# Kernel optimization log

Hardware: AMD Instinct MI355X
Metric: run time of the kernel (lower is better)

Reference implementation:

```python
import jax, jax.numpy as jnp
import numpy as np

NHEAD = 8
D_K = 64
BETA = 2.0
MIN_RBF = 0.01
MAX_RBF = 0.99
MIN_SPREAD, MAX_SPREAD, BASE, NUM_SPREAD = 1.0, 6.0, 20.0, 8
LN_EPS = 1e-5


def _spreads():
    # torch: min + (max-min) * (logspace(0,1,num,base) - 1) / (base - 1)
    return MIN_SPREAD + (MAX_SPREAD - MIN_SPREAD) * (BASE ** jnp.linspace(0.0, 1.0, NUM_SPREAD) - 1.0) / (BASE - 1.0)


def _layernorm(x, g, b):
    m = jnp.mean(x, axis=-1, keepdims=True)
    v = jnp.mean((x - m) ** 2, axis=-1, keepdims=True)
    return (x - m) * jax.lax.rsqrt(v + LN_EPS) * g + b


def setup_inputs() -> dict:
    key = jax.random.key(0)
    ks = jax.random.split(key, 12)
    B, N, D, H, K, DH = 4, 1024, 512, NHEAD, D_K, 1024
    s = 0.05
    return {
        "x": jax.random.normal(ks[0], (B, N, D), jnp.float32),
        "coords": jax.random.normal(ks[1], (B, N, 3), jnp.float32) * 8.0,  # Angstrom-scale spread
        "q_proj": jax.random.normal(ks[2], (H, D, K), jnp.float32) * s,
        "k_proj": jax.random.normal(ks[3], (H, D, K), jnp.float32) * s,
        "v_proj": jax.random.normal(ks[4], (H, D, K), jnp.float32) * s,
        "q_bias": jnp.zeros((H, K), jnp.float32),
        "k_bias": jnp.zeros((H, K), jnp.float32),
        "v_bias": jnp.zeros((H, K), jnp.float32),
        "w_out": jax.random.normal(ks[5], (D, D), jnp.float32) * s,
        "ln1_g": jnp.ones((D,), jnp.float32),
        "ln1_b": jnp.zeros((D,), jnp.float32),
        "w1": jax.random.normal(ks[6], (DH, D), jnp.float32) * s,
        "b1": jnp.zeros((DH,), jnp.float32),
        "w2": jax.random.normal(ks[7], (D, DH), jnp.float32) * s,
        "b2": jnp.zeros((D,), jnp.float32),
        "ln2_g": jnp.ones((D,), jnp.float32),
        "ln2_b": jnp.zeros((D,), jnp.float32),
    }


def reference(x, coords, q_proj, k_proj, v_proj, q_bias, k_bias, v_bias,
              w_out, ln1_g, ln1_b, w1, b1, w2, b2, ln2_g, ln2_b):
    B, N, D = x.shape
    # per-head QKV projections: [B,H,N,K]
    Q = jnp.einsum('bnd,hdk->bhnk', x, q_proj) + q_bias[None, :, None, :]
    K_ = jnp.einsum('bnd,hdk->bhnk', x, k_proj) + k_bias[None, :, None, :]
    V = jnp.einsum('bnd,hdk->bhnk', x, v_proj) + v_bias[None, :, None, :]

    S = jnp.einsum('bhnk,bhmk->bhnm', Q, K_) / np.float32(np.sqrt(D_K))

    # pairwise squared distances [B,N,N] and per-head gaussian RBFs [B,H,N,N]
    d2 = jnp.sum((coords[:, :, None, :] - coords[:, None, :, :]) ** 2, axis=-1)
    spreads = _spreads().astype(x.dtype)  # [H]
    rbf = jnp.exp(-d2[:, None, :, :] / (2.0 * spreads[None, :, None, None] ** 2))
    valid = (rbf >= MIN_RBF) & (rbf <= MAX_RBF)  # sparse attention band

    # probs proportional to exp(S) * rbf**beta, restricted to the valid band
    logits = jnp.where(valid, S + BETA * jnp.log(jnp.maximum(rbf, 1e-12)), -1e9)
    p = jax.nn.softmax(logits, axis=-1)
    p = jnp.where(valid, p, 0.0)  # fully-masked rows -> zero output

    o = jnp.einsum('bhnm,bhmk->bhnk', p, V)
    # torch: out.permute(0,2,3,1).reshape(B,N,D) -> interleave (d_k, head)
    o = o.transpose(0, 2, 3, 1).reshape(B, N, D)
    attn_out = o @ w_out.T

    x = _layernorm(x + attn_out, ln1_g, ln1_b)
    h = jax.nn.gelu(x @ w1.T + b1)
    ffn = h @ w2.T + b2
    x = _layernorm(x + ffn, ln2_g, ln2_b)
    return x
```

## Files before the change

kernel.cpp:

```cpp
#include <hip/hip_runtime.h>
#include <cmath>

typedef short s16x8 __attribute__((ext_vector_type(8)));
typedef float f32x4 __attribute__((ext_vector_type(4)));
typedef unsigned short u16;

#define MFMA(a, b, c) __builtin_amdgcn_mfma_f32_16x16x32_bf16((a), (b), (c), 0, 0, 0)
#define NEG_INF (-__builtin_inff())

__device__ inline u16 f2b(float f) {
    union { float f; unsigned u; } v; v.f = f;
    unsigned r = v.u + 0x7fffu + ((v.u >> 16) & 1u);
    return (u16)(r >> 16);
}

__device__ inline void glds16(const u16* g, u16* l) {
    __builtin_amdgcn_global_load_lds(
        (const __attribute__((address_space(1))) unsigned int*)g,
        (__attribute__((address_space(3))) unsigned int*)l, 16, 0, 0);
}

__global__ __launch_bounds__(256) void prep_kernel(
    const float* __restrict__ x,
    const float* __restrict__ qp, const float* __restrict__ kp, const float* __restrict__ vp,
    const float* __restrict__ w_out, const float* __restrict__ w1, const float* __restrict__ w2,
    u16* __restrict__ xb, u16* __restrict__ Bqkv, u16* __restrict__ w_outp,
    u16* __restrict__ w1b, u16* __restrict__ w2b)
{
    const int NXV = 262144;
    const int NQKV = 786432;
    const int NWO = 262144;
    const int NW1 = 524288;
    const int NW2 = 524288;
    const int TOT = NXV + NQKV + NWO + NW1 + NW2;
    for (int i = blockIdx.x * 256 + threadIdx.x; i < TOT; i += gridDim.x * 256) {
        int j = i;
        if (j < NXV) {
            const int base = j * 8;
            float4 a0 = *(const float4*)(x + base);
            float4 a1 = *(const float4*)(x + base + 4);
            s16x8 o;
            o[0]=f2b(a0.x); o[1]=f2b(a0.y); o[2]=f2b(a0.z); o[3]=f2b(a0.w);
            o[4]=f2b(a1.x); o[5]=f2b(a1.y); o[6]=f2b(a1.z); o[7]=f2b(a1.w);
            *(s16x8*)(xb + base) = o;
            continue;
        }
        j -= NXV;
        if (j < NQKV) {
            const int k = j & 63, d = (j >> 6) & 511, zh = j >> 15;
            const int z = zh >> 3, h = zh & 7;
            const float* W = (z == 0) ? qp : (z == 1) ? kp : vp;
            const float v = W[h * 32768 + d * 64 + k];
            Bqkv[(z * 512 + h * 64 + k) * 512 + d] = f2b(v);
            continue;
        }
        j -= NQKV;
        if (j < NWO) {
            const int oc = j & 511, row = j >> 9;
            const int h = oc >> 6, k = oc & 63;
            w_outp[j] = f2b(w_out[row * 512 + k * 8 + h]);
            continue;
        }
        j -= NWO;
        if (j < NW1) { w1b[j] = f2b(w1[j]); continue; }
        j -= NW1;
        w2b[j] = f2b(w2[j]);
    }
}

template<int TM>
__device__ inline void gemm_core(const u16* __restrict__ A, const u16* __restrict__ B,
                                 int K, int ktiles, int kstart, int r0, int c0,
                                 u16* As, u16* Bs, f32x4 (&acc)[TM / 32][4])
{
    const int t = threadIdx.x, lane = t & 63, wid = t >> 6;
    const int l15 = lane & 15, lg = lane >> 4, sw = l15 & 7;
    constexpr int FR = TM / 32;
    const int wr = (wid & 1) * (TM / 2), wc = (wid >> 1) * 64;
    constexpr int NA = TM * 8 / 256;

    const f32x4 zero = {0.f, 0.f, 0.f, 0.f};
    #pragma unroll
    for (int fr = 0; fr < FR; ++fr)
        #pragma unroll
        for (int fc = 0; fc < 4; ++fc) acc[fr][fc] = zero;

    for (int kt = 0; kt < ktiles; ++kt) {
        const int k0 = kstart + kt * 64;
        __syncthreads();
        #pragma unroll
        for (int i = 0; i < NA; ++i) {
            const int slot = i * 256 + t;
            const int row = slot >> 3, c = slot & 7;
            glds16(A + (size_t)(r0 + row) * K + k0 + ((c ^ (row & 7)) << 3),
                   As + i * 2048 + wid * 512);
        }
        #pragma unroll
        for (int i = 0; i < 4; ++i) {
            const int slot = i * 256 + t;
            const int row = slot >> 3, c = slot & 7;
            glds16(B + (size_t)(c0 + row) * K + k0 + ((c ^ (row & 7)) << 3),
                   Bs + i * 2048 + wid * 512);
        }
        __syncthreads();
        #pragma unroll
        for (int ks = 0; ks < 2; ++ks) {
            const int cc = ((ks * 4 + lg) ^ sw) * 8;
            s16x8 af[FR], bf[4];
            #pragma unroll
            for (int f = 0; f < FR; ++f)
                af[f] = *(const s16x8*)(As + (wr + f * 16 + l15) * 64 + cc);
            #pragma unroll
            for (int f = 0; f < 4; ++f)
                bf[f] = *(const s16x8*)(Bs + (wc + f * 16 + l15) * 64 + cc);
            #pragma unroll
            for (int fr = 0; fr < FR; ++fr)
                #pragma unroll
                for (int fc = 0; fc < 4; ++fc)
                    acc[fr][fc] = MFMA(af[fr], bf[fc], acc[fr][fc]);
        }
    }
}

__global__ __launch_bounds__(256) void gemm_qkv_kernel(
    const u16* __restrict__ xb, const u16* __restrict__ Bqkv,
    const float* __restrict__ qb, const float* __restrict__ kb, const float* __restrict__ vb,
    u16* __restrict__ Qb, u16* __restrict__ Kb, u16* __restrict__ Vtb)
{
    __shared__ __align__(16) u16 As[64 * 64];
    __shared__ __align__(16) u16 Bs[128 * 64];
    f32x4 acc[2][4];
    const int r0 = blockIdx.x * 64, c0 = blockIdx.y * 128;
    gemm_core<64>(xb, Bqkv, 512, 8, 0, r0, c0, As, Bs, acc);

    const int t = threadIdx.x, lane = t & 63, wid = t >> 6;
    const int wr = (wid & 1) * 32, wc = (wid >> 1) * 64;
    const int l15 = lane & 15, lg = lane >> 4;

    #pragma unroll
    for (int fc = 0; fc < 4; ++fc) {
        const int gc = c0 + wc + fc * 16 + l15;
        const int z = gc >> 9;
        const int hk = gc & 511;
        const int h = hk >> 6, k = gc & 63;
        const float bias = (z == 0 ? qb : z == 1 ? kb : vb)[hk];
        #pragma unroll
        for (int fr = 0; fr < 2; ++fr) {
            #pragma unroll
            for (int r = 0; r < 4; ++r) {
                const int grow = r0 + wr + fr * 16 + lg * 4 + r;
                const int b = grow >> 10, n = grow & 1023;
                const int bh = b * 8 + h;
                const u16 val = f2b(acc[fr][fc][r] + bias);
                if (z == 0)      Qb[(size_t)bh * 65536 + n * 64 + k] = val;
                else if (z == 1) Kb[(size_t)bh * 65536 + n * 64 + k] = val;
                else             Vtb[(size_t)bh * 65536 + k * 1024 + n] = val;
            }
        }
    }
}

template<int EPI>
__global__ __launch_bounds__(256) void gemm_kernel(
    const u16* __restrict__ A, const u16* __restrict__ B, const float* __restrict__ bias,
    float* __restrict__ Cf, u16* __restrict__ Cb, int N, int K, int ktiles, size_t pstride)
{
    __shared__ __align__(16) u16 As[64 * 64];
    __shared__ __align__(16) u16 Bs[128 * 64];
    f32x4 acc[2][4];
    const int r0 = blockIdx.x * 64, c0 = blockIdx.y * 128;
    const int kstart = blockIdx.z * ktiles * 64;
    gemm_core<64>(A, B, K, ktiles, kstart, r0, c0, As, Bs, acc);
    float* Cfz = Cf + (size_t)blockIdx.z * pstride;

    const int t = threadIdx.x, lane = t & 63, wid = t >> 6;
    const int wr = (wid & 1) * 32, wc = (wid >> 1) * 64;
    const int l15 = lane & 15, lg = lane >> 4;

    #pragma unroll
    for (int fc = 0; fc < 4; ++fc) {
        const int gc = c0 + wc + fc * 16 + l15;
        const float bv = (EPI == 2) ? bias[gc] : 0.f;
        #pragma unroll
        for (int fr = 0; fr < 2; ++fr) {
            #pragma unroll
            for (int r = 0; r < 4; ++r) {
                const int grow = r0 + wr + fr * 16 + lg * 4 + r;
                float v = acc[fr][fc][r] + bv;
                if (EPI == 2) {
                    const float u = 0.7978845608028654f * (v + 0.044715f * v * v * v);
                    v = 0.5f * v * (1.0f + tanhf(u));
                    Cb[(size_t)grow * N + gc] = f2b(v);
                } else {
                    Cfz[(size_t)grow * N + gc] = v;
                }
            }
        }
    }
}

struct AttnParams { float g[8], lo[8], hi[8]; };

__global__ __launch_bounds__(256) void attn_kernel(
    const u16* __restrict__ Qb, const u16* __restrict__ Kb, const u16* __restrict__ Vtb,
    const float* __restrict__ coords, u16* __restrict__ Ob, AttnParams prm)
{
    __shared__ float cmx[1024], cmy[1024], cmz[1024];
    __shared__ __align__(16) u16 Ps[4][16][72];

    const int wg = blockIdx.x;
    const int swz = (wg & 7) * 64 + (wg >> 3);
    const int bh = swz >> 4;
    const int n0 = (swz & 15) * 64;
    const int b = bh >> 3, h = bh & 7;
    const float g = prm.g[h], lo = prm.lo[h], hi = prm.hi[h];

    const int t = threadIdx.x, lane = t & 63, wid = t >> 6;
    const int l15 = lane & 15, lg = lane >> 4;
    const int wq0 = wid * 16;

    for (int i = t; i < 1024; i += 256) {
        const float* c = coords + ((size_t)b * 1024 + i) * 3;
        cmx[i] = c[0]; cmy[i] = c[1]; cmz[i] = c[2];
    }
    __syncthreads();

    s16x8 qf[2];
    {
        const u16* qp_ = Qb + (size_t)bh * 65536 + (size_t)(n0 + wq0 + l15) * 64;
        qf[0] = *(const s16x8*)(qp_ + lg * 8);
        qf[1] = *(const s16x8*)(qp_ + 32 + lg * 8);
    }
    float qx[4], qy[4], qz[4];
    #pragma unroll
    for (int r = 0; r < 4; ++r) {
        const int qn = n0 + wq0 + lg * 4 + r;
        qx[r] = cmx[qn]; qy[r] = cmy[qn]; qz[r] = cmz[qn];
    }

    float m_run[4], l_run[4];
    f32x4 o_acc[4];
    const f32x4 zero = {0.f, 0.f, 0.f, 0.f};
    #pragma unroll
    for (int r = 0; r < 4; ++r) { m_run[r] = NEG_INF; l_run[r] = 0.f; }
    #pragma unroll
    for (int kf = 0; kf < 4; ++kf) o_acc[kf] = zero;

    const u16* Kbh = Kb + (size_t)bh * 65536;
    const u16* Vbh = Vtb + (size_t)bh * 65536;

    for (int mt = 0; mt < 16; ++mt) {
        const int m0 = mt * 64;

        f32x4 s[4];
        #pragma unroll
        for (int mf = 0; mf < 4; ++mf) {
            const u16* kp_ = Kbh + (size_t)(m0 + mf * 16 + l15) * 64;
            s16x8 kf0 = *(const s16x8*)(kp_ + lg * 8);
            s16x8 kf1 = *(const s16x8*)(kp_ + 32 + lg * 8);
            f32x4 a = zero;
            a = MFMA(qf[0], kf0, a);
            a = MFMA(qf[1], kf1, a);
            s[mf] = a;
        }

        s16x8 vfr[2][4];
        #pragma unroll
        for (int ms = 0; ms < 2; ++ms)
            #pragma unroll
            for (int kf = 0; kf < 4; ++kf)
                vfr[ms][kf] = *(const s16x8*)(Vbh + (size_t)(kf * 16 + l15) * 1024
                                              + m0 + ms * 32 + lg * 8);

        float p[4][4];
        float tmax[4] = {NEG_INF, NEG_INF, NEG_INF, NEG_INF};
        #pragma unroll
        for (int mf = 0; mf < 4; ++mf) {
            const int mloc = m0 + mf * 16 + l15;
            const float mx = cmx[mloc], my = cmy[mloc], mz = cmz[mloc];
            #pragma unroll
            for (int r = 0; r < 4; ++r) {
                const float dx = qx[r] - mx, dy = qy[r] - my, dz = qz[r] - mz;
                const float d2 = fmaf(dx, dx, fmaf(dy, dy, dz * dz));
                const bool valid = (d2 >= lo) && (d2 <= hi);
                const float lgt = fmaf(s[mf][r], 0.125f, d2 * g);
                const float v = valid ? lgt : NEG_INF;
                p[mf][r] = v;
                tmax[r] = fmaxf(tmax[r], v);
            }
        }
        #pragma unroll
        for (int r = 0; r < 4; ++r) {
            float v = tmax[r];
            v = fmaxf(v, __shfl_xor(v, 1));
            v = fmaxf(v, __shfl_xor(v, 2));
            v = fmaxf(v, __shfl_xor(v, 4));
            v = fmaxf(v, __shfl_xor(v, 8));
            const float mnew = fmaxf(m_run[r], v);
            const float scale = (mnew == NEG_INF) ? 1.f : __expf(m_run[r] - mnew);
            m_run[r] = mnew;
            float rs = 0.f;
            #pragma unroll
            for (int mf = 0; mf < 4; ++mf) {
                const float pv = (p[mf][r] == NEG_INF) ? 0.f : __expf(p[mf][r] - mnew);
                p[mf][r] = pv;
                rs += pv;
            }
            rs += __shfl_xor(rs, 1); rs += __shfl_xor(rs, 2);
            rs += __shfl_xor(rs, 4); rs += __shfl_xor(rs, 8);
            l_run[r] = l_run[r] * scale + rs;
            #pragma unroll
            for (int kf = 0; kf < 4; ++kf) o_acc[kf][r] *= scale;
        }

        #pragma unroll
        for (int mf = 0; mf < 4; ++mf)
            #pragma unroll
            for (int r = 0; r < 4; ++r)
                Ps[wid][lg * 4 + r][mf * 16 + l15] = f2b(p[mf][r]);

        #pragma unroll
        for (int ms = 0; ms < 2; ++ms) {
            s16x8 pa = *(const s16x8*)&Ps[wid][l15][ms * 32 + lg * 8];
            #pragma unroll
            for (int kf = 0; kf < 4; ++kf)
                o_acc[kf] = MFMA(pa, vfr[ms][kf], o_acc[kf]);
        }
    }

    #pragma unroll
    for (int kf = 0; kf < 4; ++kf) {
        #pragma unroll
        for (int r = 0; r < 4; ++r) {
            const int n = n0 + wq0 + lg * 4 + r;
            const float invl = (l_run[r] > 0.f) ? 1.f / l_run[r] : 0.f;
            Ob[((size_t)b * 1024 + n) * 512 + h * 64 + kf * 16 + l15] = f2b(o_acc[kf][r] * invl);
        }
    }
}

template<int NSRC, bool CB, bool WB16>
__global__ __launch_bounds__(256) void add_ln_kernel(
    const float* __restrict__ a, const float* __restrict__ b0, const float* __restrict__ b1,
    const float* __restrict__ cb, const float* __restrict__ g, const float* __restrict__ bt,
    float* __restrict__ out, u16* __restrict__ outb)
{
    const int lane = threadIdx.x & 63;
    const int row = blockIdx.x * 4 + (threadIdx.x >> 6);
    const size_t base = (size_t)row * 512 + lane * 8;

    float v[8];
    {
        float4 a0 = *(const float4*)(a + base);
        float4 a1 = *(const float4*)(a + base + 4);
        float4 p0 = *(const float4*)(b0 + base);
        float4 p1 = *(const float4*)(b0 + base + 4);
        v[0]=a0.x+p0.x; v[1]=a0.y+p0.y; v[2]=a0.z+p0.z; v[3]=a0.w+p0.w;
        v[4]=a1.x+p1.x; v[5]=a1.y+p1.y; v[6]=a1.z+p1.z; v[7]=a1.w+p1.w;
        if (NSRC == 3) {
            float4 q0 = *(const float4*)(b1 + base);
            float4 q1 = *(const float4*)(b1 + base + 4);
            v[0]+=q0.x; v[1]+=q0.y; v[2]+=q0.z; v[3]+=q0.w;
            v[4]+=q1.x; v[5]+=q1.y; v[6]+=q1.z; v[7]+=q1.w;
        }
        if (CB) {
            float4 c0 = *(const float4*)(cb + lane * 8);
            float4 c1 = *(const float4*)(cb + lane * 8 + 4);
            v[0]+=c0.x; v[1]+=c0.y; v[2]+=c0.z; v[3]+=c0.w;
            v[4]+=c1.x; v[5]+=c1.y; v[6]+=c1.z; v[7]+=c1.w;
        }
    }
    float s = 0.f;
    #pragma unroll
    for (int k = 0; k < 8; ++k) s += v[k];
    #pragma unroll
    for (int m = 1; m <= 32; m <<= 1) s += __shfl_xor(s, m);
    const float mean = s * (1.0f / 512.0f);

    float vs = 0.f;
    #pragma unroll
    for (int k = 0; k < 8; ++k) { const float d = v[k] - mean; vs += d * d; }
    #pragma unroll
    for (int m = 1; m <= 32; m <<= 1) vs += __shfl_xor(vs, m);
    const float rstd = rsqrtf(vs * (1.0f / 512.0f) + 1e-5f);

    float4 g0 = *(const float4*)(g + lane * 8);
    float4 g1 = *(const float4*)(g + lane * 8 + 4);
    float4 t0 = *(const float4*)(bt + lane * 8);
    float4 t1 = *(const float4*)(bt + lane * 8 + 4);
    float gg[8] = {g0.x,g0.y,g0.z,g0.w,g1.x,g1.y,g1.z,g1.w};
    float tb[8] = {t0.x,t0.y,t0.z,t0.w,t1.x,t1.y,t1.z,t1.w};

    float o[8];
    #pragma unroll
    for (int k = 0; k < 8; ++k) o[k] = (v[k] - mean) * rstd * gg[k] + tb[k];
    float4 w0; w0.x=o[0]; w0.y=o[1]; w0.z=o[2]; w0.w=o[3];
    float4 w1; w1.x=o[4]; w1.y=o[5]; w1.z=o[6]; w1.w=o[7];
    *(float4*)(out + base) = w0;
    *(float4*)(out + base + 4) = w1;
    if (WB16) {
        s16x8 q;
        #pragma unroll
        for (int k = 0; k < 8; ++k) q[k] = (short)f2b(o[k]);
        *(s16x8*)(outb + base) = q;
    }
}

extern "C" void kernel_launch(void* const* d_in, const int* in_sizes, int n_in,
                              void* d_out, int out_size, void* d_ws, size_t ws_size,
                              hipStream_t stream)
{
    const float* x      = (const float*)d_in[0];
    const float* coords = (const float*)d_in[1];
    const float* qp     = (const float*)d_in[2];
    const float* kp     = (const float*)d_in[3];
    const float* vp     = (const float*)d_in[4];
    const float* qbias  = (const float*)d_in[5];
    const float* kbias  = (const float*)d_in[6];
    const float* vbias  = (const float*)d_in[7];
    const float* w_out  = (const float*)d_in[8];
    const float* ln1g   = (const float*)d_in[9];
    const float* ln1b   = (const float*)d_in[10];
    const float* w1     = (const float*)d_in[11];
    const float* b1     = (const float*)d_in[12];
    const float* w2     = (const float*)d_in[13];
    const float* b2     = (const float*)d_in[14];
    const float* ln2g   = (const float*)d_in[15];
    const float* ln2b   = (const float*)d_in[16];
    float* out = (float*)d_out;

    char* W = (char*)d_ws;
    u16*  xb     = (u16*)(W + 0);
    u16*  Bqkv   = (u16*)(W + 4194304);
    u16*  w_outp = (u16*)(W + 5767168);
    u16*  w1b    = (u16*)(W + 6291456);
    u16*  w2b    = (u16*)(W + 7340032);
    u16*  Qb     = (u16*)(W + 8388608);
    u16*  Kb     = (u16*)(W + 12582912);
    u16*  Vtb    = (u16*)(W + 16777216);
    u16*  Ob     = (u16*)(W + 20971520);
    float* X1    = (float*)(W + 25165824);
    u16*  Hb     = (u16*)(W + 33554432);
    float* P0    = (float*)(W + 41943040);
    float* P1    = P0 + 2097152;
    u16*  X1b    = Qb;

    AttnParams prm;
    for (int h = 0; h < 8; ++h) {
        const double sg = 1.0 + 5.0 * (pow(20.0, (double)h / 7.0) - 1.0) / 19.0;
        const double s2 = sg * sg;
        prm.g[h]  = (float)(-1.0 / s2);
        prm.lo[h] = (float)(2.0 * s2 * log(100.0 / 99.0));
        prm.hi[h] = (float)(2.0 * s2 * log(100.0));
    }

    prep_kernel<<<1024, 256, 0, stream>>>(x, qp, kp, vp, w_out, w1, w2,
                                          xb, Bqkv, w_outp, w1b, w2b);
    gemm_qkv_kernel<<<dim3(64, 12), 256, 0, stream>>>(xb, Bqkv, qbias, kbias, vbias,
                                                      Qb, Kb, Vtb);
    attn_kernel<<<512, 256, 0, stream>>>(Qb, Kb, Vtb, coords, Ob, prm);
    gemm_kernel<0><<<dim3(64, 4, 2), 256, 0, stream>>>(Ob, w_outp, nullptr, P0, nullptr,
                                                       512, 512, 4, 2097152);
    add_ln_kernel<3, false, true><<<1024, 256, 0, stream>>>(x, P0, P1, nullptr,
                                                            ln1g, ln1b, X1, X1b);
    gemm_kernel<2><<<dim3(64, 8), 256, 0, stream>>>(X1b, w1b, b1, nullptr, Hb,
                                                    1024, 512, 8, 0);
    gemm_kernel<0><<<dim3(64, 4, 2), 256, 0, stream>>>(Hb, w2b, nullptr, P0, nullptr,
                                                       512, 1024, 8, 2097152);
    add_ln_kernel<3, true, false><<<1024, 256, 0, stream>>>(X1, P0, P1, b2,
                                                            ln2g, ln2b, out, nullptr);
}
```

Measured before the change: 138.7 us.

## Split attention over key halves, drop online-max softmax, enlarge GEMM tiles

The attention kernel is split into two key-range halves, which doubles the block count to 1024. Each half writes unnormalised fp32 partial outputs and row sums, and a new merge kernel combines them into bf16. The online running-max softmax is replaced by exp2 with a fixed offset of -8, and the 1/sqrt(dk)·log2e scale is folded into Q in the QKV GEMM epilogue. This removes the per-tile max reductions, rescaling and shuffles. Separately, all GEMMs move from 64-row to 128-row tiles (4x4 MFMA fragments per wave), which gives more reuse but halves the grid. The fixed-offset softmax relies on logits staying in a bounded range and may overflow or underflow for larger-magnitude inputs. The split adds an extra kernel and fp32 partial traffic.

New measurement: 166.8 us. 20.2% more time.

```diff
diff --git a/kernel.cpp b/kernel.cpp
--- a/kernel.cpp
+++ b/kernel.cpp
@@ -68,20 +68,17 @@
     }
 }
 
-template<int TM>
 __device__ inline void gemm_core(const u16* __restrict__ A, const u16* __restrict__ B,
                                  int K, int ktiles, int kstart, int r0, int c0,
-                                 u16* As, u16* Bs, f32x4 (&acc)[TM / 32][4])
+                                 u16* As, u16* Bs, f32x4 (&acc)[4][4])
 {
     const int t = threadIdx.x, lane = t & 63, wid = t >> 6;
     const int l15 = lane & 15, lg = lane >> 4, sw = l15 & 7;
-    constexpr int FR = TM / 32;
-    const int wr = (wid & 1) * (TM / 2), wc = (wid >> 1) * 64;
-    constexpr int NA = TM * 8 / 256;
+    const int wr = (wid & 1) * 64, wc = (wid >> 1) * 64;
 
     const f32x4 zero = {0.f, 0.f, 0.f, 0.f};
     #pragma unroll
-    for (int fr = 0; fr < FR; ++fr)
+    for (int fr = 0; fr < 4; ++fr)
         #pragma unroll
         for (int fc = 0; fc < 4; ++fc) acc[fr][fc] = zero;
 
@@ -89,7 +86,7 @@
         const int k0 = kstart + kt * 64;
         __syncthreads();
         #pragma unroll
-        for (int i = 0; i < NA; ++i) {
+        for (int i = 0; i < 4; ++i) {
             const int slot = i * 256 + t;
             const int row = slot >> 3, c = slot & 7;
             glds16(A + (size_t)(r0 + row) * K + k0 + ((c ^ (row & 7)) << 3),
@@ -106,15 +103,15 @@
         #pragma unroll
         for (int ks = 0; ks < 2; ++ks) {
             const int cc = ((ks * 4 + lg) ^ sw) * 8;
-            s16x8 af[FR], bf[4];
-            #pragma unroll
-            for (int f = 0; f < FR; ++f)
+            s16x8 af[4], bf[4];
+            #pragma unroll
+            for (int f = 0; f < 4; ++f)
                 af[f] = *(const s16x8*)(As + (wr + f * 16 + l15) * 64 + cc);
             #pragma unroll
             for (int f = 0; f < 4; ++f)
                 bf[f] = *(const s16x8*)(Bs + (wc + f * 16 + l15) * 64 + cc);
             #pragma unroll
-            for (int fr = 0; fr < FR; ++fr)
+            for (int fr = 0; fr < 4; ++fr)
                 #pragma unroll
                 for (int fc = 0; fc < 4; ++fc)
                     acc[fr][fc] = MFMA(af[fr], bf[fc], acc[fr][fc]);
@@ -122,19 +119,20 @@
     }
 }
 
+#define SCALE_Q 0.18033688f
 __global__ __launch_bounds__(256) void gemm_qkv_kernel(
     const u16* __restrict__ xb, const u16* __restrict__ Bqkv,
     const float* __restrict__ qb, const float* __restrict__ kb, const float* __restrict__ vb,
     u16* __restrict__ Qb, u16* __restrict__ Kb, u16* __restrict__ Vtb)
 {
-    __shared__ __align__(16) u16 As[64 * 64];
+    __shared__ __align__(16) u16 As[128 * 64];
     __shared__ __align__(16) u16 Bs[128 * 64];
-    f32x4 acc[2][4];
-    const int r0 = blockIdx.x * 64, c0 = blockIdx.y * 128;
-    gemm_core<64>(xb, Bqkv, 512, 8, 0, r0, c0, As, Bs, acc);
+    f32x4 acc[4][4];
+    const int r0 = blockIdx.x * 128, c0 = blockIdx.y * 128;
+    gemm_core(xb, Bqkv, 512, 8, 0, r0, c0, As, Bs, acc);
 
     const int t = threadIdx.x, lane = t & 63, wid = t >> 6;
-    const int wr = (wid & 1) * 32, wc = (wid >> 1) * 64;
+    const int wr = (wid & 1) * 64, wc = (wid >> 1) * 64;
     const int l15 = lane & 15, lg = lane >> 4;
 
     #pragma unroll
@@ -145,13 +143,15 @@
         const int h = hk >> 6, k = gc & 63;
         const float bias = (z == 0 ? qb : z == 1 ? kb : vb)[hk];
         #pragma unroll
-        for (int fr = 0; fr < 2; ++fr) {
+        for (int fr = 0; fr < 4; ++fr) {
             #pragma unroll
             for (int r = 0; r < 4; ++r) {
                 const int grow = r0 + wr + fr * 16 + lg * 4 + r;
                 const int b = grow >> 10, n = grow & 1023;
                 const int bh = b * 8 + h;
-                const u16 val = f2b(acc[fr][fc][r] + bias);
+                float v = acc[fr][fc][r] + bias;
+                if (z == 0) v *= SCALE_Q;
+                const u16 val = f2b(v);
                 if (z == 0)      Qb[(size_t)bh * 65536 + n * 64 + k] = val;
                 else if (z == 1) Kb[(size_t)bh * 65536 + n * 64 + k] = val;
                 else             Vtb[(size_t)bh * 65536 + k * 1024 + n] = val;
@@ -165,16 +165,16 @@
     const u16* __restrict__ A, const u16* __restrict__ B, const float* __restrict__ bias,
     float* __restrict__ Cf, u16* __restrict__ Cb, int N, int K, int ktiles, size_t pstride)
 {
-    __shared__ __align__(16) u16 As[64 * 64];
+    __shared__ __align__(16) u16 As[128 * 64];
     __shared__ __align__(16) u16 Bs[128 * 64];
-    f32x4 acc[2][4];
-    const int r0 = blockIdx.x * 64, c0 = blockIdx.y * 128;
+    f32x4 acc[4][4];
+    const int r0 = blockIdx.x * 128, c0 = blockIdx.y * 128;
     const int kstart = blockIdx.z * ktiles * 64;
-    gemm_core<64>(A, B, K, ktiles, kstart, r0, c0, As, Bs, acc);
+    gemm_core(A, B, K, ktiles, kstart, r0, c0, As, Bs, acc);
     float* Cfz = Cf + (size_t)blockIdx.z * pstride;
 
     const int t = threadIdx.x, lane = t & 63, wid = t >> 6;
-    const int wr = (wid & 1) * 32, wc = (wid >> 1) * 64;
+    const int wr = (wid & 1) * 64, wc = (wid >> 1) * 64;
     const int l15 = lane & 15, lg = lane >> 4;
 
     #pragma unroll
@@ -182,7 +182,7 @@
         const int gc = c0 + wc + fc * 16 + l15;
         const float bv = (EPI == 2) ? bias[gc] : 0.f;
         #pragma unroll
-        for (int fr = 0; fr < 2; ++fr) {
+        for (int fr = 0; fr < 4; ++fr) {
             #pragma unroll
             for (int r = 0; r < 4; ++r) {
                 const int grow = r0 + wr + fr * 16 + lg * 4 + r;
@@ -199,21 +199,24 @@
     }
 }
 
-struct AttnParams { float g[8], lo[8], hi[8]; };
-
-__global__ __launch_bounds__(256) void attn_kernel(
+struct AttnParams { float g2[8], lo[8], hi[8]; };
+
+__global__ __launch_bounds__(256, 4) void attn_kernel(
     const u16* __restrict__ Qb, const u16* __restrict__ Kb, const u16* __restrict__ Vtb,
-    const float* __restrict__ coords, u16* __restrict__ Ob, AttnParams prm)
+    const float* __restrict__ coords, float* __restrict__ Po, float* __restrict__ Lo,
+    AttnParams prm)
 {
     __shared__ float cmx[1024], cmy[1024], cmz[1024];
     __shared__ __align__(16) u16 Ps[4][16][72];
 
     const int wg = blockIdx.x;
-    const int swz = (wg & 7) * 64 + (wg >> 3);
-    const int bh = swz >> 4;
-    const int n0 = (swz & 15) * 64;
+    const int swz = (wg & 7) * 128 + (wg >> 3);
+    const int bh = swz >> 5;
+    const int rest = swz & 31;
+    const int n0 = (rest >> 1) * 64;
+    const int z = rest & 1;
     const int b = bh >> 3, h = bh & 7;
-    const float g = prm.g[h], lo = prm.lo[h], hi = prm.hi[h];
+    const float g2 = prm.g2[h], lo = prm.lo[h], hi = prm.hi[h];
 
     const int t = threadIdx.x, lane = t & 63, wid = t >> 6;
     const int l15 = lane & 15, lg = lane >> 4;
@@ -238,18 +241,17 @@
         qx[r] = cmx[qn]; qy[r] = cmy[qn]; qz[r] = cmz[qn];
     }
 
-    float m_run[4], l_run[4];
     f32x4 o_acc[4];
     const f32x4 zero = {0.f, 0.f, 0.f, 0.f};
-    #pragma unroll
-    for (int r = 0; r < 4; ++r) { m_run[r] = NEG_INF; l_run[r] = 0.f; }
+    float l_lane[4] = {0.f, 0.f, 0.f, 0.f};
     #pragma unroll
     for (int kf = 0; kf < 4; ++kf) o_acc[kf] = zero;
 
     const u16* Kbh = Kb + (size_t)bh * 65536;
     const u16* Vbh = Vtb + (size_t)bh * 65536;
 
-    for (int mt = 0; mt < 16; ++mt) {
+    const int mt0 = z * 8;
+    for (int mt = mt0; mt < mt0 + 8; ++mt) {
         const int m0 = mt * 64;
 
         f32x4 s[4];
@@ -272,8 +274,6 @@
                 vfr[ms][kf] = *(const s16x8*)(Vbh + (size_t)(kf * 16 + l15) * 1024
                                               + m0 + ms * 32 + lg * 8);
 
-        float p[4][4];
-        float tmax[4] = {NEG_INF, NEG_INF, NEG_INF, NEG_INF};
         #pragma unroll
         for (int mf = 0; mf < 4; ++mf) {
             const int mloc = m0 + mf * 16 + l15;
@@ -283,41 +283,12 @@
                 const float dx = qx[r] - mx, dy = qy[r] - my, dz = qz[r] - mz;
                 const float d2 = fmaf(dx, dx, fmaf(dy, dy, dz * dz));
                 const bool valid = (d2 >= lo) && (d2 <= hi);
-                const float lgt = fmaf(s[mf][r], 0.125f, d2 * g);
-                const float v = valid ? lgt : NEG_INF;
-                p[mf][r] = v;
-                tmax[r] = fmaxf(tmax[r], v);
+                float pv = exp2f(fmaf(d2, g2, s[mf][r]) - 8.0f);
+                pv = valid ? pv : 0.f;
+                l_lane[r] += pv;
+                Ps[wid][lg * 4 + r][mf * 16 + l15] = f2b(pv);
             }
         }
-        #pragma unroll
-        for (int r = 0; r < 4; ++r) {
-            float v = tmax[r];
-            v = fmaxf(v, __shfl_xor(v, 1));
-            v = fmaxf(v, __shfl_xor(v, 2));
-            v = fmaxf(v, __shfl_xor(v, 4));
-            v = fmaxf(v, __shfl_xor(v, 8));
-            const float mnew = fmaxf(m_run[r], v);
-            const float scale = (mnew == NEG_INF) ? 1.f : __expf(m_run[r] - mnew);
-            m_run[r] = mnew;
-            float rs = 0.f;
-            #pragma unroll
-            for (int mf = 0; mf < 4; ++mf) {
-                const float pv = (p[mf][r] == NEG_INF) ? 0.f : __expf(p[mf][r] - mnew);
-                p[mf][r] = pv;
-                rs += pv;
-            }
-            rs += __shfl_xor(rs, 1); rs += __shfl_xor(rs, 2);
-            rs += __shfl_xor(rs, 4); rs += __shfl_xor(rs, 8);
-            l_run[r] = l_run[r] * scale + rs;
-            #pragma unroll
-            for (int kf = 0; kf < 4; ++kf) o_acc[kf][r] *= scale;
-        }
-
-        #pragma unroll
-        for (int mf = 0; mf < 4; ++mf)
-            #pragma unroll
-            for (int r = 0; r < 4; ++r)
-                Ps[wid][lg * 4 + r][mf * 16 + l15] = f2b(p[mf][r]);
 
         #pragma unroll
         for (int ms = 0; ms < 2; ++ms) {
@@ -329,17 +300,58 @@
     }
 
     #pragma unroll
-    for (int kf = 0; kf < 4; ++kf) {
+    for (int r = 0; r < 4; ++r) {
+        float v = l_lane[r];
+        v += __shfl_xor(v, 1); v += __shfl_xor(v, 2);
+        v += __shfl_xor(v, 4); v += __shfl_xor(v, 8);
+        l_lane[r] = v;
+    }
+
+    float* PoZ = Po + (size_t)(z * 32 + bh) * 65536;
+    #pragma unroll
+    for (int kf = 0; kf < 4; ++kf)
         #pragma unroll
         for (int r = 0; r < 4; ++r) {
             const int n = n0 + wq0 + lg * 4 + r;
-            const float invl = (l_run[r] > 0.f) ? 1.f / l_run[r] : 0.f;
-            Ob[((size_t)b * 1024 + n) * 512 + h * 64 + kf * 16 + l15] = f2b(o_acc[kf][r] * invl);
-        }
-    }
-}
-
-template<int NSRC, bool CB, bool WB16>
+            PoZ[(size_t)n * 64 + kf * 16 + l15] = o_acc[kf][r];
+        }
+    if (l15 == 0) {
+        #pragma unroll
+        for (int r = 0; r < 4; ++r)
+            Lo[z * 32768 + bh * 1024 + n0 + wq0 + lg * 4 + r] = l_lane[r];
+    }
+}
+
+__global__ __launch_bounds__(256) void attn_merge_kernel(
+    const float* __restrict__ Po, const float* __restrict__ Lo, u16* __restrict__ Ob)
+{
+    const int gid = blockIdx.x * 256 + threadIdx.x;
+    const int row = gid >> 3;
+    const int k0 = (gid & 7) * 8;
+    const int bh = row >> 10, n = row & 1023;
+    const int b = bh >> 3, h = bh & 7;
+    const float l0 = Lo[row], l1 = Lo[32768 + row];
+    const float lt = l0 + l1;
+    const float invl = (lt > 0.f) ? 1.f / lt : 0.f;
+    const float* p0 = Po + (size_t)row * 64 + k0;
+    const float* p1 = Po + 2097152 + (size_t)row * 64 + k0;
+    float4 a0 = *(const float4*)p0;
+    float4 a1 = *(const float4*)(p0 + 4);
+    float4 b0 = *(const float4*)p1;
+    float4 b1 = *(const float4*)(p1 + 4);
+    s16x8 o;
+    o[0] = f2b((a0.x + b0.x) * invl);
+    o[1] = f2b((a0.y + b0.y) * invl);
+    o[2] = f2b((a0.z + b0.z) * invl);
+    o[3] = f2b((a0.w + b0.w) * invl);
+    o[4] = f2b((a1.x + b1.x) * invl);
+    o[5] = f2b((a1.y + b1.y) * invl);
+    o[6] = f2b((a1.z + b1.z) * invl);
+    o[7] = f2b((a1.w + b1.w) * invl);
+    *(s16x8*)(Ob + ((size_t)b * 1024 + n) * 512 + h * 64 + k0) = o;
+}
+
+template<bool CB, bool WB16>
 __global__ __launch_bounds__(256) void add_ln_kernel(
     const float* __restrict__ a, const float* __restrict__ b0, const float* __restrict__ b1,
     const float* __restrict__ cb, const float* __restrict__ g, const float* __restrict__ bt,
@@ -357,12 +369,10 @@
         float4 p1 = *(const float4*)(b0 + base + 4);
         v[0]=a0.x+p0.x; v[1]=a0.y+p0.y; v[2]=a0.z+p0.z; v[3]=a0.w+p0.w;
         v[4]=a1.x+p1.x; v[5]=a1.y+p1.y; v[6]=a1.z+p1.z; v[7]=a1.w+p1.w;
-        if (NSRC == 3) {
-            float4 q0 = *(const float4*)(b1 + base);
-            float4 q1 = *(const float4*)(b1 + base + 4);
-            v[0]+=q0.x; v[1]+=q0.y; v[2]+=q0.z; v[3]+=q0.w;
-            v[4]+=q1.x; v[5]+=q1.y; v[6]+=q1.z; v[7]+=q1.w;
-        }
+        float4 q0 = *(const float4*)(b1 + base);
+        float4 q1 = *(const float4*)(b1 + base + 4);
+        v[0]+=q0.x; v[1]+=q0.y; v[2]+=q0.z; v[3]+=q0.w;
+        v[4]+=q1.x; v[5]+=q1.y; v[6]+=q1.z; v[7]+=q1.w;
         if (CB) {
             float4 c0 = *(const float4*)(cb + lane * 8);
             float4 c1 = *(const float4*)(cb + lane * 8 + 4);
@@ -444,29 +454,32 @@
     float* P0    = (float*)(W + 41943040);
     float* P1    = P0 + 2097152;
     u16*  X1b    = Qb;
+    float* Po    = P0;
+    float* Lo    = X1;
 
     AttnParams prm;
     for (int h = 0; h < 8; ++h) {
         const double sg = 1.0 + 5.0 * (pow(20.0, (double)h / 7.0) - 1.0) / 19.0;
         const double s2 = sg * sg;
-        prm.g[h]  = (float)(-1.0 / s2);
+        prm.g2[h] = (float)(-1.4426950408889634 / s2);
         prm.lo[h] = (float)(2.0 * s2 * log(100.0 / 99.0));
         prm.hi[h] = (float)(2.0 * s2 * log(100.0));
     }
 
     prep_kernel<<<1024, 256, 0, stream>>>(x, qp, kp, vp, w_out, w1, w2,
                                           xb, Bqkv, w_outp, w1b, w2b);
-    gemm_qkv_kernel<<<dim3(64, 12), 256, 0, stream>>>(xb, Bqkv, qbias, kbias, vbias,
+    gemm_qkv_kernel<<<dim3(32, 12), 256, 0, stream>>>(xb, Bqkv, qbias, kbias, vbias,
                                                       Qb, Kb, Vtb);
-    attn_kernel<<<512, 256, 0, stream>>>(Qb, Kb, Vtb, coords, Ob, prm);
-    gemm_kernel<0><<<dim3(64, 4, 2), 256, 0, stream>>>(Ob, w_outp, nullptr, P0, nullptr,
+    attn_kernel<<<1024, 256, 0, stream>>>(Qb, Kb, Vtb, coords, Po, Lo, prm);
+    attn_merge_kernel<<<1024, 256, 0, stream>>>(Po, Lo, Ob);
+    gemm_kernel<0><<<dim3(32, 4, 2), 256, 0, stream>>>(Ob, w_outp, nullptr, P0, nullptr,
                                                        512, 512, 4, 2097152);
-    add_ln_kernel<3, false, true><<<1024, 256, 0, stream>>>(x, P0, P1, nullptr,
-                                                            ln1g, ln1b, X1, X1b);
-    gemm_kernel<2><<<dim3(64, 8), 256, 0, stream>>>(X1b, w1b, b1, nullptr, Hb,
+    add_ln_kernel<false, true><<<1024, 256, 0, stream>>>(x, P0, P1, nullptr,
+                                                         ln1g, ln1b, X1, X1b);
+    gemm_kernel<2><<<dim3(32, 8), 256, 0, stream>>>(X1b, w1b, b1, nullptr, Hb,
                                                     1024, 512, 8, 0);
-    gemm_kernel<0><<<dim3(64, 4, 2), 256, 0, stream>>>(Hb, w2b, nullptr, P0, nullptr,
+    gemm_kernel<0><<<dim3(32, 4, 2), 256, 0, stream>>>(Hb, w2b, nullptr, P0, nullptr,
                                                        512, 1024, 8, 2097152);
-    add_ln_kernel<3, true, false><<<1024, 256, 0, stream>>>(X1, P0, P1, b2,
-                                                            ln2g, ln2b, out, nullptr);
-}
+    add_ln_kernel<true, false><<<1024, 256, 0, stream>>>(X1, P0, P1, b2,
+                                                         ln2g, ln2b, out, nullptr);
+}
```
